# Kernel tuning notes

Measured on AMD Instinct MI355X. Metric: run time of the kernel, lower is better.

The kernel has to match this reference:

```python
import jax, jax.numpy as jnp
import numpy as np

NUM_HEADS = 16
GROUP_SIZE = 4
RMS_EPS = 1e-6


def _rope_cos_sin(S, head_dim):
    # matches compute_freqs_cis: freqs = 1/10000**(arange(0,hd,2)/hd), angles = outer(t, freqs)
    inv_freq = 1.0 / (10000.0 ** (jnp.arange(0, head_dim, 2, dtype=jnp.float32) / head_dim))
    t = jnp.arange(S, dtype=jnp.float32)
    angles = t[:, None] * inv_freq[None, :]          # [S, hd/2]
    return jnp.cos(angles), jnp.sin(angles)


def _apply_rope(x, cos, sin):
    # x: [B, S, h, hd]; complex multiply on (even, odd) pairs
    B, S, h, hd = x.shape
    xr = x.reshape(B, S, h, hd // 2, 2)
    x0, x1 = xr[..., 0], xr[..., 1]
    c = cos[None, :, None, :]
    s = sin[None, :, None, :]
    o0 = x0 * c - x1 * s
    o1 = x0 * s + x1 * c
    return jnp.stack([o0, o1], axis=-1).reshape(B, S, h, hd)


def setup_inputs() -> dict:
    key = jax.random.key(0)
    k1, k2, k3 = jax.random.split(key, 3)
    B, S, H = 4, 2048, 2048
    g = GROUP_SIZE
    x = jax.random.normal(k1, (B, S, H), dtype=jnp.float32)
    w_attn = jax.random.normal(k2, (H, H + 2 * H // g), dtype=jnp.float32) * 0.02
    w_proj = jax.random.normal(k3, (H, H), dtype=jnp.float32) * 0.02
    norm_w = jnp.ones((H,), dtype=jnp.float32)
    return {"x": x, "w_attn": w_attn, "w_proj": w_proj, "norm_w": norm_w}


def reference(x, w_attn, w_proj, norm_w):
    B, S, H = x.shape
    nh = NUM_HEADS
    g = GROUP_SIZE
    nkv = nh // g
    hd = H // nh
    ghd = H // g

    qkv = jnp.einsum('bsh,hf->bsf', x, w_attn)
    q = qkv[..., :H].reshape(B, S, nh, hd)
    k = qkv[..., H:H + ghd].reshape(B, S, nkv, hd)
    v = qkv[..., H + ghd:].reshape(B, S, nkv, hd)

    cos, sin = _rope_cos_sin(S, hd)
    q = _apply_rope(q, cos, sin)
    k = _apply_rope(k, cos, sin)

    q = q.transpose(0, 2, 1, 3)                      # [B, nh, S, hd]
    k = jnp.repeat(k.transpose(0, 2, 1, 3), g, axis=1)   # [B, nh, S, hd]
    v = jnp.repeat(v.transpose(0, 2, 1, 3), g, axis=1)

    scale = 1.0 / jnp.sqrt(jnp.float32(hd))
    scores = jnp.einsum('bhqd,bhkd->bhqk', q, k) * scale
    causal = jnp.tril(jnp.ones((S, S), dtype=bool))
    scores = jnp.where(causal[None, None], scores, jnp.finfo(scores.dtype).min)
    attn = jax.nn.softmax(scores, axis=-1)
    y = jnp.einsum('bhqk,bhkd->bhqd', attn, v)       # [B, nh, S, hd]
    y = y.transpose(0, 2, 1, 3).reshape(B, S, H)

    y = jnp.einsum('bsh,ho->bso', y, w_proj)
    # RMSNorm
    rms = jnp.sqrt(jnp.mean(jnp.square(y), axis=-1, keepdims=True) + RMS_EPS)
    return (y / rms) * norm_w
```

## Files before the change

kernel.cpp:

```cpp
#include <hip/hip_runtime.h>

#define DEVI __device__ __forceinline__

using u16 = unsigned short;
using u32 = unsigned int;

typedef __attribute__((ext_vector_type(8))) short short8v;
typedef __attribute__((ext_vector_type(4))) float f32x4;
typedef __attribute__((ext_vector_type(16))) float f32x16;
typedef __attribute__((ext_vector_type(2))) u32 u32x2;
typedef __attribute__((ext_vector_type(4))) u32 u32x4;

DEVI u16 f2b(float f) {
  u32 u = __builtin_bit_cast(u32, f);
  u += 0x7fffu + ((u >> 16) & 1u);
  return (u16)(u >> 16);
}
DEVI float b2f(u16 b) { return __builtin_bit_cast(float, (u32)b << 16); }

DEVI void gload16(const void* g, void* l) {
  __builtin_amdgcn_global_load_lds(
      (const __attribute__((address_space(1))) void*)g,
      (__attribute__((address_space(3))) void*)l, 16, 0, 0);
}

__global__ __launch_bounds__(256) void cvt_x_k(const float* __restrict__ in,
                                               u16* __restrict__ out) {
  size_t i = ((size_t)blockIdx.x * 256 + threadIdx.x) * 8;
  f32x4 a = *(const f32x4*)(in + i);
  f32x4 c = *(const f32x4*)(in + i + 4);
  short8v o;
  o[0] = (short)f2b(a[0]); o[1] = (short)f2b(a[1]);
  o[2] = (short)f2b(a[2]); o[3] = (short)f2b(a[3]);
  o[4] = (short)f2b(c[0]); o[5] = (short)f2b(c[1]);
  o[6] = (short)f2b(c[2]); o[7] = (short)f2b(c[3]);
  *(short8v*)(out + i) = o;
}

__global__ __launch_bounds__(256) void transpose_cvt_k(
    const float* __restrict__ in, u16* __restrict__ out, int R, int Ccols) {
  __shared__ u16 tile[64][65];
  const int r0 = blockIdx.y * 64, c0 = blockIdx.x * 64;
  const int tx = threadIdx.x & 63, ty = threadIdx.x >> 6;
#pragma unroll
  for (int jj = 0; jj < 16; ++jj) {
    int r = ty + jj * 4;
    tile[r][tx] = f2b(in[(size_t)(r0 + r) * Ccols + c0 + tx]);
  }
  __syncthreads();
#pragma unroll
  for (int jj = 0; jj < 16; ++jj) {
    int c = ty + jj * 4;
    out[(size_t)(c0 + c) * R + r0 + tx] = tile[tx][c];
  }
}

__global__ __launch_bounds__(256) void rope_table_k(float* __restrict__ cosT,
                                                    float* __restrict__ sinT) {
  int idx = blockIdx.x * 256 + threadIdx.x;
  int s = idx >> 6, i = idx & 63;
  float inv_freq = expf(-(float)i * (1.0f / 64.0f) * 9.210340371976184f);
  float ang = (float)s * inv_freq;
  cosT[idx] = cosf(ang);
  sinT[idx] = sinf(ang);
}

__global__ __launch_bounds__(256) void rope_scatter_k(
    const u16* __restrict__ qkv, const float* __restrict__ cosT,
    const float* __restrict__ sinT, u16* __restrict__ q_r,
    u16* __restrict__ k_r) {
  const float QS = 0.08838834764831845f * 1.4426950408889634f;
  const int row = blockIdx.x;
  const int b = row >> 11, s = row & 2047;
  const u16* in = qkv + (size_t)row * 3072;
  const float* cp = cosT + s * 64;
  const float* sp = sinT + s * 64;
  for (int p = threadIdx.x; p < 1280; p += 256) {
    int f0 = p * 2;
    u32 pair = *(const u32*)(in + f0);
    float x0 = b2f((u16)(pair & 0xffffu));
    float x1 = b2f((u16)(pair >> 16));
    int d, head;
    u16* dst;
    bool isq = (f0 < 2048);
    if (isq) {
      head = f0 >> 7; d = f0 & 127;
      dst = q_r + (((size_t)(b * 16 + head)) * 2048 + s) * 128 + d;
    } else {
      int idx = f0 - 2048;
      head = idx >> 7; d = idx & 127;
      dst = k_r + (((size_t)(b * 4 + head)) * 2048 + s) * 128 + d;
    }
    int i = d >> 1;
    float c = cp[i], sn = sp[i];
    float o0 = x0 * c - x1 * sn;
    float o1 = x0 * sn + x1 * c;
    if (isq) { o0 *= QS; o1 *= QS; }
    *(u32*)dst = (u32)f2b(o0) | ((u32)f2b(o1) << 16);
  }
}

__global__ __launch_bounds__(256) void v_trans_k(const u16* __restrict__ qkv,
                                                 u16* __restrict__ vT) {
  __shared__ u16 tile[64][65];
  const int s0 = blockIdx.x * 64, d0 = blockIdx.y * 64;
  const int bk = blockIdx.z;
  const int b = bk >> 2, kh = bk & 3;
  const int tx = threadIdx.x & 63, ty = threadIdx.x >> 6;
  const u16* src = qkv + ((size_t)b * 2048) * 3072 + 2560 + kh * 128;
#pragma unroll
  for (int jj = 0; jj < 16; ++jj) {
    int s = ty + jj * 4;
    tile[s][tx] = src[(size_t)(s0 + s) * 3072 + d0 + tx];
  }
  __syncthreads();
  u16* dst = vT + (((size_t)bk * 128 + d0) * 2048) + s0;
#pragma unroll
  for (int jj = 0; jj < 16; ++jj) {
    int dd = ty + jj * 4;
    dst[(size_t)dd * 2048 + tx] = tile[tx][dd];
  }
}

DEVI short8v ldf(const char* half, int r, int slot) {
  return *(const short8v*)(half + r * 64 + (((slot) ^ (r & 3)) << 4));
}

DEVI void stg(const u16* __restrict__ G, int row0, int Kd, int T, int kh,
              char* dst, int t, int w) {
#pragma unroll
  for (int i = 0; i < 2; ++i) {
    int off = i * 8192 + t * 16;
    int r = off >> 6;
    int gs = ((off >> 4) & 3) ^ (r & 3);
    gload16((const char*)G +
                (((size_t)(row0 + r) * Kd) + T * 64 + kh * 32 + gs * 8) * 2,
            dst + i * 8192 + w * 1024);
  }
}

#define VM4 asm volatile("s_waitcnt vmcnt(4)" ::: "memory")
#define PH(P2, KS, CH, STAGE_STMT, TAILWAIT)                                   \
  {                                                                            \
    if ((CH) == 0) {                                                           \
      _Pragma("unroll") for (int mt = 0; mt < 8; ++mt) af[mt] =                \
          ldf(Ab + (P2) * 32768 + (KS) * 16384, wm * 128 + mt * 16 + lo, hi);  \
    }                                                                          \
    bf0 = ldf(Bb + (P2) * 32768 + (KS) * 16384, wn * 64 + (CH) * 32 + lo, hi);\
    bf1 = ldf(Bb + (P2) * 32768 + (KS) * 16384,                                \
              wn * 64 + (CH) * 32 + 16 + lo, hi);                              \
    STAGE_STMT;                                                                \
    __builtin_amdgcn_sched_barrier(0);                                         \
    __builtin_amdgcn_s_barrier();                                              \
    asm volatile("s_waitcnt lgkmcnt(0)" ::: "memory");                         \
    __builtin_amdgcn_sched_barrier(0);                                         \
    __builtin_amdgcn_s_setprio(1);                                             \
    _Pragma("unroll") for (int mt = 0; mt < 8; ++mt) {                         \
      acc[mt][(CH) * 2] = __builtin_amdgcn_mfma_f32_16x16x32_bf16(             \
          af[mt], bf0, acc[mt][(CH) * 2], 0, 0, 0);                            \
      acc[mt][(CH) * 2 + 1] = __builtin_amdgcn_mfma_f32_16x16x32_bf16(         \
          af[mt], bf1, acc[mt][(CH) * 2 + 1], 0, 0, 0);                        \
    }                                                                          \
    __builtin_amdgcn_s_setprio(0);                                             \
    TAILWAIT;                                                                  \
    __builtin_amdgcn_sched_barrier(0);                                         \
    __builtin_amdgcn_s_barrier();                                              \
    __builtin_amdgcn_sched_barrier(0);                                         \
  }

__global__ __launch_bounds__(512, 2) void gemm256_k(const u16* __restrict__ A,
                                                    const u16* __restrict__ BT,
                                                    u16* __restrict__ C, int N,
                                                    int Kd) {
  __shared__ __align__(16) char lds[131072];
  char* Ab = lds;
  char* Bb = lds + 65536;

  const int t = threadIdx.x;
  const int lane = t & 63, lo = lane & 15, hi = lane >> 4;
  const int w = t >> 6, wm = w >> 2, wn = w & 3;

  const int ntx = gridDim.x;
  const int nwg = ntx * gridDim.y;
  const int orig = blockIdx.y * ntx + blockIdx.x;
  const int cpx = nwg >> 3;
  const int swz = (orig & 7) * cpx + (orig >> 3);
  const int m0 = (swz / ntx) * 256, n0 = (swz % ntx) * 256;

  f32x4 acc[8][4];
#pragma unroll
  for (int a = 0; a < 8; ++a)
#pragma unroll
    for (int c = 0; c < 4; ++c) acc[a][c] = (f32x4){0.f, 0.f, 0.f, 0.f};

  short8v af[8], bf0, bf1;

  const int NK = Kd >> 6;
  const int NK2 = NK >> 1;

  stg(A, m0, Kd, 0, 0, Ab + 0, t, w);
  stg(BT, n0, Kd, 0, 0, Bb + 0, t, w);
  stg(A, m0, Kd, 0, 1, Ab + 16384, t, w);
  stg(BT, n0, Kd, 0, 1, Bb + 16384, t, w);
  stg(A, m0, Kd, 1, 0, Ab + 32768, t, w);
  stg(BT, n0, Kd, 1, 0, Bb + 32768, t, w);
  VM4;
  __builtin_amdgcn_sched_barrier(0);
  __builtin_amdgcn_s_barrier();
  __builtin_amdgcn_sched_barrier(0);

  for (int kt2 = 0; kt2 < NK2; ++kt2) {
    int T1v = 2 * kt2 + 1;
    int T2v = 2 * kt2 + 2; if (T2v > NK - 1) T2v = NK - 1;
    int T3v = 2 * kt2 + 3; if (T3v > NK - 1) T3v = NK - 1;
    PH(0, 0, 0, stg(A, m0, Kd, T1v, 1, Ab + 49152, t, w), (void)0);
    PH(0, 0, 1, stg(BT, n0, Kd, T1v, 1, Bb + 49152, t, w), (void)0);
    PH(0, 1, 0, stg(A, m0, Kd, T2v, 0, Ab + 0, t, w), (void)0);
    PH(0, 1, 1, stg(BT, n0, Kd, T2v, 0, Bb + 0, t, w), VM4);
    PH(1, 0, 0, stg(A, m0, Kd, T2v, 1, Ab + 16384, t, w), (void)0);
    PH(1, 0, 1, stg(BT, n0, Kd, T2v, 1, Bb + 16384, t, w), (void)0);
    PH(1, 1, 0, stg(A, m0, Kd, T3v, 0, Ab + 32768, t, w), (void)0);
    PH(1, 1, 1, stg(BT, n0, Kd, T3v, 0, Bb + 32768, t, w), VM4);
  }
  asm volatile("s_waitcnt vmcnt(0)" ::: "memory");

#pragma unroll
  for (int mt = 0; mt < 8; ++mt)
#pragma unroll
    for (int nt = 0; nt < 4; ++nt)
#pragma unroll
      for (int r = 0; r < 4; ++r) {
        int row = m0 + wm * 128 + mt * 16 + hi * 4 + r;
        int col = n0 + wn * 64 + nt * 16 + lo;
        C[(size_t)row * N + col] = f2b(acc[mt][nt][r]);
      }
}

__global__ __launch_bounds__(256, 2) void attn_k(const u16* __restrict__ Q,
                                                 const u16* __restrict__ K,
                                                 const u16* __restrict__ VT,
                                                 u16* __restrict__ Y) {
  __shared__ __align__(16) u16 lK[2][64 * 128];
  __shared__ __align__(16) u16 lV[2][128 * 64];

  const int t = threadIdx.x;
  const int lane = t & 63;
  const int l31 = lane & 31, hb = lane >> 5;
  const int w = t >> 6;

  const int id = blockIdx.x;
  const int xcd = id & 7, pos = id >> 3;
  const int bh = xcd + ((pos >> 4) << 3);
  const int qt = 15 - (pos & 15);
  const int b = bh >> 4, h = bh & 15, kh = h >> 2;

  const size_t qbase = (size_t)(b * 16 + h) * 2048 * 128;
  const size_t kbase = (size_t)(b * 4 + kh) * 2048 * 128;
  const size_t vbase = (size_t)(b * 4 + kh) * 128 * 2048;

  const int q0 = qt * 128;
  const int qrow = q0 + w * 32 + l31;

  short8v qf[8];
#pragma unroll
  for (int j16 = 0; j16 < 8; ++j16)
    qf[j16] = *(const short8v*)(Q + qbase + (size_t)qrow * 128 + j16 * 16 + hb * 8);

  float m_run = -3.0e38f, l_run = 0.f;
  f32x16 oacc[4];
#pragma unroll
  for (int db = 0; db < 4; ++db)
#pragma unroll
    for (int rg = 0; rg < 16; ++rg) oacc[db][rg] = 0.f;

  const int ntile = 2 * qt + 2;

  auto stage = [&](int buf, int j) {
    const int kv0 = j * 64;
#pragma unroll
    for (int i = 0; i < 4; ++i) {
      int off = i * 4096 + t * 16;
      int r = off >> 8;
      int sl = (off >> 4) & 15;
      int gs = sl ^ (r & 7);
      gload16((const char*)K + (kbase + (size_t)(kv0 + r) * 128 + gs * 8) * 2,
              (char*)lK[buf] + i * 4096 + w * 1024);
    }
#pragma unroll
    for (int i = 0; i < 4; ++i) {
      int off = i * 4096 + t * 16;
      int r = off >> 7;
      int sl = (off >> 4) & 7;
      int gs = sl ^ (r & 7);
      gload16((const char*)VT + (vbase + (size_t)r * 2048 + kv0 + gs * 8) * 2,
              (char*)lV[buf] + i * 4096 + w * 1024);
    }
  };

  stage(0, 0);
  __syncthreads();

  for (int jj = 0; jj < ntile; ++jj) {
    const int cur = jj & 1;
    if (jj + 1 < ntile) stage(cur ^ 1, jj + 1);

    const char* lKc = (const char*)lK[cur];
    const char* lVc = (const char*)lV[cur];
    const int kv0 = jj * 64;

    f32x16 sacc[2];
#pragma unroll
    for (int kb = 0; kb < 2; ++kb)
#pragma unroll
      for (int rg = 0; rg < 16; ++rg) sacc[kb][rg] = 0.f;

    __builtin_amdgcn_s_setprio(1);
#pragma unroll
    for (int j16 = 0; j16 < 8; ++j16) {
      const int c = j16 * 2 + hb;
#pragma unroll
      for (int kb = 0; kb < 2; ++kb) {
        int kr = kb * 32 + l31;
        short8v kf = *(const short8v*)(lKc + kr * 256 + ((c ^ (kr & 7)) << 4));
        sacc[kb] = __builtin_amdgcn_mfma_f32_32x32x16_bf16(kf, qf[j16],
                                                           sacc[kb], 0, 0, 0);
      }
    }
    __builtin_amdgcn_s_setprio(0);

    if (jj >= ntile - 2) {
      const int mb = kv0 + 4 * hb - qrow;
#pragma unroll
      for (int kb = 0; kb < 2; ++kb)
#pragma unroll
        for (int rg = 0; rg < 16; ++rg)
          if (mb + kb * 32 + (rg & 3) + 8 * (rg >> 2) > 0)
            sacc[kb][rg] = -1.0e38f;
    }

    float mx = sacc[0][0];
#pragma unroll
    for (int rg = 1; rg < 16; ++rg) mx = fmaxf(mx, sacc[0][rg]);
#pragma unroll
    for (int rg = 0; rg < 16; ++rg) mx = fmaxf(mx, sacc[1][rg]);
    mx = fmaxf(mx, __shfl_xor(mx, 32, 64));

    if (__any(mx > m_run + 8.f)) {
      float mn = fmaxf(m_run, mx);
      float corr = exp2f(m_run - mn);
      m_run = mn;
      l_run *= corr;
#pragma unroll
      for (int db = 0; db < 4; ++db)
#pragma unroll
        for (int rg = 0; rg < 16; ++rg) oacc[db][rg] *= corr;
    }

    float sm = 0.f;
#pragma unroll
    for (int kb = 0; kb < 2; ++kb)
#pragma unroll
      for (int rg = 0; rg < 16; ++rg) {
        float p = exp2f(sacc[kb][rg] - m_run);
        sacc[kb][rg] = p;
        sm += p;
      }
    sm += __shfl_xor(sm, 32, 64);
    l_run += sm;

    short8v pa[4];
#pragma unroll
    for (int kb = 0; kb < 2; ++kb) {
      u32 pw00, pw01, pw10, pw11, pw20, pw21, pw30, pw31;
      asm("v_cvt_pk_bf16_f32 %0, %1, %2" : "=v"(pw00) : "v"(sacc[kb][0]), "v"(sacc[kb][1]));
      asm("v_cvt_pk_bf16_f32 %0, %1, %2" : "=v"(pw01) : "v"(sacc[kb][2]), "v"(sacc[kb][3]));
      asm("v_cvt_pk_bf16_f32 %0, %1, %2" : "=v"(pw10) : "v"(sacc[kb][4]), "v"(sacc[kb][5]));
      asm("v_cvt_pk_bf16_f32 %0, %1, %2" : "=v"(pw11) : "v"(sacc[kb][6]), "v"(sacc[kb][7]));
      asm("v_cvt_pk_bf16_f32 %0, %1, %2" : "=v"(pw20) : "v"(sacc[kb][8]), "v"(sacc[kb][9]));
      asm("v_cvt_pk_bf16_f32 %0, %1, %2" : "=v"(pw21) : "v"(sacc[kb][10]), "v"(sacc[kb][11]));
      asm("v_cvt_pk_bf16_f32 %0, %1, %2" : "=v"(pw30) : "v"(sacc[kb][12]), "v"(sacc[kb][13]));
      asm("v_cvt_pk_bf16_f32 %0, %1, %2" : "=v"(pw31) : "v"(sacc[kb][14]), "v"(sacc[kb][15]));
      u32x2 a0 = __builtin_amdgcn_permlane32_swap(pw00, pw10, false, false);
      u32x2 a1 = __builtin_amdgcn_permlane32_swap(pw01, pw11, false, false);
      u32x4 wv0; wv0[0] = a0[0]; wv0[1] = a1[0]; wv0[2] = a0[1]; wv0[3] = a1[1];
      pa[kb * 2 + 0] = __builtin_bit_cast(short8v, wv0);
      u32x2 b0 = __builtin_amdgcn_permlane32_swap(pw20, pw30, false, false);
      u32x2 b1 = __builtin_amdgcn_permlane32_swap(pw21, pw31, false, false);
      u32x4 wv1; wv1[0] = b0[0]; wv1[1] = b1[0]; wv1[2] = b0[1]; wv1[3] = b1[1];
      pa[kb * 2 + 1] = __builtin_bit_cast(short8v, wv1);
    }

    __builtin_amdgcn_s_setprio(1);
#pragma unroll
    for (int sc = 0; sc < 4; ++sc) {
      const int c = sc * 2 + hb;
#pragma unroll
      for (int db = 0; db < 4; ++db) {
        int vr = db * 32 + l31;
        short8v vf = *(const short8v*)(lVc + vr * 128 + ((c ^ (vr & 7)) << 4));
        oacc[db] = __builtin_amdgcn_mfma_f32_32x32x16_bf16(vf, pa[sc],
                                                           oacc[db], 0, 0, 0);
      }
    }
    __builtin_amdgcn_s_setprio(0);

    __syncthreads();
  }

  const float inv = 1.0f / l_run;
  u16* yp = Y + ((size_t)b * 2048 + qrow) * 2048 + h * 128;
#pragma unroll
  for (int db = 0; db < 4; ++db)
#pragma unroll
    for (int j = 0; j < 4; ++j) {
      float a0 = oacc[db][4 * j] * inv, a1 = oacc[db][4 * j + 1] * inv;
      float a2 = oacc[db][4 * j + 2] * inv, a3 = oacc[db][4 * j + 3] * inv;
      u32 w0, w1;
      asm("v_cvt_pk_bf16_f32 %0, %1, %2" : "=v"(w0) : "v"(a0), "v"(a1));
      asm("v_cvt_pk_bf16_f32 %0, %1, %2" : "=v"(w1) : "v"(a2), "v"(a3));
      *(u32x2*)(yp + db * 32 + 8 * j + 4 * hb) = (u32x2){w0, w1};
    }
}

__global__ __launch_bounds__(256) void rmsnorm_k(const u16* __restrict__ Yb,
                                                 const float* __restrict__ nw,
                                                 float* __restrict__ out) {
  const int row = blockIdx.x;
  const int t = threadIdx.x;
  const u16* yr = Yb + (size_t)row * 2048 + t * 8;
  short8v v = *(const short8v*)yr;
  float x[8];
  float ss = 0.f;
#pragma unroll
  for (int j = 0; j < 8; ++j) {
    x[j] = b2f((u16)v[j]);
    ss += x[j] * x[j];
  }
#pragma unroll
  for (int dm = 1; dm < 64; dm <<= 1) ss += __shfl_xor(ss, dm, 64);
  __shared__ float red[4];
  if ((t & 63) == 0) red[t >> 6] = ss;
  __syncthreads();
  float tot = red[0] + red[1] + red[2] + red[3];
  float inv = rsqrtf(tot * (1.0f / 2048.0f) + 1e-6f);
  float* op = out + (size_t)row * 2048 + t * 8;
  const float* wp = nw + t * 8;
  f32x4 o0, o1;
#pragma unroll
  for (int j = 0; j < 4; ++j) o0[j] = x[j] * inv * wp[j];
#pragma unroll
  for (int j = 0; j < 4; ++j) o1[j] = x[4 + j] * inv * wp[4 + j];
  *(f32x4*)op = o0;
  *(f32x4*)(op + 4) = o1;
}

extern "C" void kernel_launch(void* const* d_in, const int* in_sizes, int n_in,
                              void* d_out, int out_size, void* d_ws,
                              size_t ws_size, hipStream_t stream) {
  (void)in_sizes; (void)n_in; (void)out_size; (void)ws_size;
  const float* x = (const float*)d_in[0];
  const float* w_attn = (const float*)d_in[1];
  const float* w_proj = (const float*)d_in[2];
  const float* norm_w = (const float*)d_in[3];
  float* out = (float*)d_out;
  char* ws = (char*)d_ws;

  size_t off = 0;
  auto alloc = [&](size_t n) {
    size_t r = off;
    off += (n + 255) & ~(size_t)255;
    return r;
  };
  u16* xb = (u16*)(ws + alloc(33554432));
  u16* wabT = (u16*)(ws + alloc(12582912));
  u16* qkv = (u16*)(ws + alloc(50331648));
  u16* q_r = (u16*)(ws + alloc(33554432));
  u16* vT = (u16*)(ws + alloc(8388608));
  u16* wpT = (u16*)(ws + alloc(8388608));
  float* cosT = (float*)(ws + alloc(524288));
  float* sinT = (float*)(ws + alloc(524288));
  u16* k_r = wabT;
  u16* y = xb;
  u16* y2 = qkv;

  cvt_x_k<<<8192, 256, 0, stream>>>(x, xb);
  transpose_cvt_k<<<dim3(48, 32), 256, 0, stream>>>(w_attn, wabT, 2048, 3072);
  transpose_cvt_k<<<dim3(32, 32), 256, 0, stream>>>(w_proj, wpT, 2048, 2048);
  rope_table_k<<<512, 256, 0, stream>>>(cosT, sinT);
  gemm256_k<<<dim3(12, 32), 512, 0, stream>>>(xb, wabT, qkv, 3072, 2048);
  rope_scatter_k<<<8192, 256, 0, stream>>>(qkv, cosT, sinT, q_r, k_r);
  v_trans_k<<<dim3(32, 2, 16), 256, 0, stream>>>(qkv, vT);
  attn_k<<<dim3(1024), 256, 0, stream>>>(q_r, k_r, vT, y);
  gemm256_k<<<dim3(8, 32), 512, 0, stream>>>(y, wpT, y2, 2048, 2048);
  rmsnorm_k<<<8192, 256, 0, stream>>>(y2, norm_w, out);
}
```

Baseline: 404.5 us.

## Single-buffer V in attention to fit three blocks per CU

Shrinks the attention kernel's LDS by single-buffering the V tile and raises launch bounds from 2 to 3 blocks per CU. V for the next tile is now loaded only after the PV MMAs finish, and explicit vmcnt waits plus barriers order the K and V loads. The max and sum reductions are also rewritten as tree reductions to shorten dependency chains. The V load is no longer overlapped with compute within a block, and the tighter register budget risks spills. The intent is that higher occupancy hides that latency instead.

```diff
diff --git a/kernel.cpp b/kernel.cpp
--- a/kernel.cpp
+++ b/kernel.cpp
@@ -236,12 +236,12 @@
       }
 }
 
-__global__ __launch_bounds__(256, 2) void attn_k(const u16* __restrict__ Q,
+__global__ __launch_bounds__(256, 3) void attn_k(const u16* __restrict__ Q,
                                                  const u16* __restrict__ K,
                                                  const u16* __restrict__ VT,
                                                  u16* __restrict__ Y) {
   __shared__ __align__(16) u16 lK[2][64 * 128];
-  __shared__ __align__(16) u16 lV[2][128 * 64];
+  __shared__ __align__(16) u16 lV[128 * 64];
 
   const int t = threadIdx.x;
   const int lane = t & 63;
@@ -275,7 +275,7 @@
 
   const int ntile = 2 * qt + 2;
 
-  auto stage = [&](int buf, int j) {
+  auto stageK = [&](int buf, int j) {
     const int kv0 = j * 64;
 #pragma unroll
     for (int i = 0; i < 4; ++i) {
@@ -286,6 +286,9 @@
       gload16((const char*)K + (kbase + (size_t)(kv0 + r) * 128 + gs * 8) * 2,
               (char*)lK[buf] + i * 4096 + w * 1024);
     }
+  };
+  auto stageV = [&](int j) {
+    const int kv0 = j * 64;
 #pragma unroll
     for (int i = 0; i < 4; ++i) {
       int off = i * 4096 + t * 16;
@@ -293,19 +296,23 @@
       int sl = (off >> 4) & 7;
       int gs = sl ^ (r & 7);
       gload16((const char*)VT + (vbase + (size_t)r * 2048 + kv0 + gs * 8) * 2,
-              (char*)lV[buf] + i * 4096 + w * 1024);
+              (char*)lV + i * 4096 + w * 1024);
     }
   };
 
-  stage(0, 0);
-  __syncthreads();
+  stageK(0, 0);
+  stageV(0);
+  asm volatile("s_waitcnt vmcnt(0)" ::: "memory");
+  __builtin_amdgcn_sched_barrier(0);
+  __builtin_amdgcn_s_barrier();
+  __builtin_amdgcn_sched_barrier(0);
 
   for (int jj = 0; jj < ntile; ++jj) {
     const int cur = jj & 1;
-    if (jj + 1 < ntile) stage(cur ^ 1, jj + 1);
+    const bool pre = (jj + 1 < ntile);
+    if (pre) stageK(cur ^ 1, jj + 1);
 
     const char* lKc = (const char*)lK[cur];
-    const char* lVc = (const char*)lV[cur];
     const int kv0 = jj * 64;
 
     f32x16 sacc[2];
@@ -338,11 +345,14 @@
             sacc[kb][rg] = -1.0e38f;
     }
 
-    float mx = sacc[0][0];
-#pragma unroll
-    for (int rg = 1; rg < 16; ++rg) mx = fmaxf(mx, sacc[0][rg]);
-#pragma unroll
-    for (int rg = 0; rg < 16; ++rg) mx = fmaxf(mx, sacc[1][rg]);
+    float mt0[16];
+#pragma unroll
+    for (int rg = 0; rg < 16; ++rg) mt0[rg] = fmaxf(sacc[0][rg], sacc[1][rg]);
+#pragma unroll
+    for (int rg = 0; rg < 8; ++rg) mt0[rg] = fmaxf(mt0[rg], mt0[rg + 8]);
+#pragma unroll
+    for (int rg = 0; rg < 4; ++rg) mt0[rg] = fmaxf(mt0[rg], mt0[rg + 4]);
+    float mx = fmaxf(fmaxf(mt0[0], mt0[1]), fmaxf(mt0[2], mt0[3]));
     mx = fmaxf(mx, __shfl_xor(mx, 32, 64));
 
     if (__any(mx > m_run + 8.f)) {
@@ -356,15 +366,19 @@
         for (int rg = 0; rg < 16; ++rg) oacc[db][rg] *= corr;
     }
 
-    float sm = 0.f;
+    float sm0[16];
 #pragma unroll
     for (int kb = 0; kb < 2; ++kb)
 #pragma unroll
-      for (int rg = 0; rg < 16; ++rg) {
-        float p = exp2f(sacc[kb][rg] - m_run);
-        sacc[kb][rg] = p;
-        sm += p;
-      }
+      for (int rg = 0; rg < 16; ++rg)
+        sacc[kb][rg] = exp2f(sacc[kb][rg] - m_run);
+#pragma unroll
+    for (int rg = 0; rg < 16; ++rg) sm0[rg] = sacc[0][rg] + sacc[1][rg];
+#pragma unroll
+    for (int rg = 0; rg < 8; ++rg) sm0[rg] += sm0[rg + 8];
+#pragma unroll
+    for (int rg = 0; rg < 4; ++rg) sm0[rg] += sm0[rg + 4];
+    float sm = (sm0[0] + sm0[1]) + (sm0[2] + sm0[3]);
     sm += __shfl_xor(sm, 32, 64);
     l_run += sm;
 
@@ -390,6 +404,12 @@
       pa[kb * 2 + 1] = __builtin_bit_cast(short8v, wv1);
     }
 
+    if (pre) { asm volatile("s_waitcnt vmcnt(4)" ::: "memory"); }
+    else     { asm volatile("s_waitcnt vmcnt(0)" ::: "memory"); }
+    __builtin_amdgcn_sched_barrier(0);
+    __builtin_amdgcn_s_barrier();
+    __builtin_amdgcn_sched_barrier(0);
+
     __builtin_amdgcn_s_setprio(1);
 #pragma unroll
     for (int sc = 0; sc < 4; ++sc) {
@@ -397,14 +417,20 @@
 #pragma unroll
       for (int db = 0; db < 4; ++db) {
         int vr = db * 32 + l31;
-        short8v vf = *(const short8v*)(lVc + vr * 128 + ((c ^ (vr & 7)) << 4));
+        short8v vf = *(const short8v*)((const char*)lV + vr * 128 +
+                                       ((c ^ (vr & 7)) << 4));
         oacc[db] = __builtin_amdgcn_mfma_f32_32x32x16_bf16(vf, pa[sc],
                                                            oacc[db], 0, 0, 0);
       }
     }
     __builtin_amdgcn_s_setprio(0);
 
-    __syncthreads();
+    asm volatile("s_waitcnt vmcnt(0)" ::: "memory");
+    __builtin_amdgcn_sched_barrier(0);
+    __builtin_amdgcn_s_barrier();
+    __builtin_amdgcn_sched_barrier(0);
+
+    if (pre) stageV(jj + 1);
   }
 
   const float inv = 1.0f / l_run;
@@ -487,7 +513,7 @@
   transpose_cvt_k<<<dim3(48, 32), 256, 0, stream>>>(w_attn, wabT, 2048, 3072);
   transpose_cvt_k<<<dim3(32, 32), 256, 0, stream>>>(w_proj, wpT, 2048, 2048);
   rope_table_k<<<512, 256, 0, stream>>>(cosT, sinT);
-  gemm256_k<<<dim3(12, 32), 512, 0, stream>>>(xb, wabT, qkv, 3072, 2048);
+  gemm256_k<<<dim3(12, 32), 512, 0, stream>>>(xb, wabT, qkv, 8192 == 0 ? 0 : 3072, 2048);
   rope_scatter_k<<<8192, 256, 0, stream>>>(qkv, cosT, sinT, q_r, k_r);
   v_trans_k<<<dim3(32, 2, 16), 256, 0, stream>>>(qkv, vT);
   attn_k<<<dim3(1024), 256, 0, stream>>>(q_r, k_r, vT, y);
```

Measured after the change: 415.4 us. 1.03x slower.
